# Performance work log

Measured on AMD Instinct MI355X. Metric: run time of the kernel, lower is better.

The kernel has to match this reference:

```python
import jax, jax.numpy as jnp
import numpy as np
from jax import lax

EPS = 1e-5

def _groupnorm1(v, scale, bias):
    # GroupNorm(1, C) on [bs, C] vectors (spatial dims are 1x1): normalize over C per sample
    m = jnp.mean(v, axis=-1, keepdims=True)
    var = jnp.mean((v - m) ** 2, axis=-1, keepdims=True)
    return (v - m) / jnp.sqrt(var + EPS) * scale + bias

def _mish(v):
    return v * jnp.tanh(jax.nn.softplus(v))


def setup_inputs() -> dict:
    key = jax.random.key(0)
    ks = jax.random.split(key, 5)
    bs, C, H, W = 32, 128, 64, 64
    K, red = 4, 16
    hid = C // red
    return {
        "x": jax.random.normal(ks[0], (bs, C, H, W), jnp.float32),
        "weight": jax.random.normal(ks[1], (K, C, C, 3, 3), jnp.float32) * 0.05,
        "bias": jax.random.normal(ks[2], (K, C), jnp.float32) * 0.05,
        "se_w1": jax.random.normal(ks[3], (hid, C), jnp.float32) * 0.1,
        "gn1_scale": jnp.ones((hid,), jnp.float32),
        "gn1_bias": jnp.zeros((hid,), jnp.float32),
        "se_w2": jax.random.normal(ks[4], (K, hid), jnp.float32) * 0.1,
        "gn2_scale": jnp.ones((K,), jnp.float32),
        "gn2_bias": jnp.zeros((K,), jnp.float32),
    }


def reference(x, weight, bias, se_w1, gn1_scale, gn1_bias, se_w2, gn2_scale, gn2_bias):
    bs, C, H, W = x.shape
    K, out_p, in_p, kh, kw = weight.shape

    # --- SqueezeAndExcitation attention -> [bs, K] in (0,1) ---
    pooled = jnp.mean(x, axis=(2, 3))                       # [bs, C]
    h1 = pooled @ se_w1.T                                   # [bs, hid] (1x1 conv, no bias)
    h1 = _mish(_groupnorm1(h1, gn1_scale, gn1_bias))
    h2 = h1 @ se_w2.T                                       # [bs, K]
    att = jax.nn.sigmoid(_groupnorm1(h2, gn2_scale, gn2_bias))

    # --- per-sample kernel / bias aggregation ---
    agg_w = jnp.einsum('bk,koihw->boihw', att, weight)      # [bs, out, in, kh, kw]
    agg_b = att @ bias                                      # [bs, out]

    # --- per-sample conv2d (equivalent to groups=bs grouped conv in torch) ---
    pad = ((1, 1), (1, 1))
    def per_sample(xi, wi):
        return lax.conv_general_dilated(
            xi[None], wi, window_strides=(1, 1), padding=pad,
            dimension_numbers=('NCHW', 'OIHW', 'NCHW'))[0]
    out = jax.vmap(per_sample)(x, agg_w)                    # [bs, out, H, W]
    return out + agg_b[:, :, None, None]
```

## Files before the change

kernel.cpp:

```cpp
#include <hip/hip_runtime.h>
#include <hip/hip_bf16.h>
#include <math.h>
#include <stdint.h>

#define EPS 1e-5f

typedef __attribute__((ext_vector_type(8))) short bf16x8;
typedef __attribute__((ext_vector_type(16))) float f32x16;

__device__ __forceinline__ ushort f2bf(float f) {
    union { float f; unsigned u; } v; v.f = f;
    unsigned r = (v.u + 0x7FFFu + ((v.u >> 16) & 1u)) >> 16;
    return (ushort)r;
}

__device__ __forceinline__ void dma16(const void* g, void* l) {
    __builtin_amdgcn_global_load_lds(
        (__attribute__((address_space(1))) const void*)(uintptr_t)g,
        (__attribute__((address_space(3))) void*)(uintptr_t)l,
        16, 0, 0);
}

__global__ __launch_bounds__(256) void transpose_kernel(const float* __restrict__ x,
                                                        ushort* __restrict__ xT,
                                                        float* __restrict__ pooled) {
    __shared__ float T[128][68];
    int bid = blockIdx.x;
    int b = (bid & 7) * 4 + (bid >> 9);
    int y = (bid >> 3) & 63;
    int t = threadIdx.x;

    int ic2 = t >> 1, half = t & 1;
    const float4* src = (const float4*)(x + (((size_t)b * 128 + ic2) * 64 + y) * 64 + half * 32);
    float4* trow = (float4*)&T[ic2][half * 32];
    float s = 0.f;
#pragma unroll
    for (int i = 0; i < 8; ++i) {
        float4 v = src[i];
        trow[i] = v;
        s += v.x + v.y + v.z + v.w;
    }
    s += __shfl_xor(s, 1, 64);
    if (half == 0) atomicAdd(&pooled[b * 128 + ic2], s * (1.0f / 4096.0f));
    __syncthreads();

    int col = t >> 2, icq = t & 3;
    uint pk[16];
#pragma unroll
    for (int jj = 0; jj < 16; ++jj) {
        float f0 = T[icq * 32 + 2 * jj][col];
        float f1 = T[icq * 32 + 2 * jj + 1][col];
        pk[jj] = (uint)f2bf(f0) | ((uint)f2bf(f1) << 16);
    }
    ushort* dst = xT + (((size_t)(b * 66 + y + 1)) * 66 + col + 1) * 128 + icq * 32;
    ((uint4*)dst)[0] = make_uint4(pk[0], pk[1], pk[2], pk[3]);
    ((uint4*)dst)[1] = make_uint4(pk[4], pk[5], pk[6], pk[7]);
    ((uint4*)dst)[2] = make_uint4(pk[8], pk[9], pk[10], pk[11]);
    ((uint4*)dst)[3] = make_uint4(pk[12], pk[13], pk[14], pk[15]);

    uint4 z = make_uint4(0, 0, 0, 0);
    if (y == 0) {
        uint4* row0 = (uint4*)(xT + ((size_t)b * 66 + 0) * 66 * 128);
        for (int i = t; i < 1056; i += 256) row0[i] = z;
    }
    if (y == 63) {
        uint4* row65 = (uint4*)(xT + ((size_t)b * 66 + 65) * 66 * 128);
        for (int i = t; i < 1056; i += 256) row65[i] = z;
    }
    if (t < 32) {
        int c = (t >> 4) * 65;
        int i = t & 15;
        *(uint4*)(xT + (((size_t)(b * 66 + y + 1)) * 66 + c) * 128 + i * 8) = z;
    }
}

__global__ __launch_bounds__(256) void aggw_kernel(const float* __restrict__ weight,
                                                   const float* __restrict__ pooled,
                                                   const float* __restrict__ se_w1,
                                                   const float* __restrict__ gn1_s, const float* __restrict__ gn1_b,
                                                   const float* __restrict__ se_w2,
                                                   const float* __restrict__ gn2_s, const float* __restrict__ gn2_b,
                                                   float* __restrict__ att_out,
                                                   ushort* __restrict__ aggw) {
    __shared__ float pl[8][128];
    __shared__ float h1s[8][8];
    __shared__ float att_s[8][4];
    int blk = blockIdx.x;
    int rep = blk / 72;
    int t = threadIdx.x;

#pragma unroll
    for (int u = 0; u < 4; ++u) {
        int pid = u * 256 + t;
        int bl = pid >> 7, ic = pid & 127;
        pl[bl][ic] = pooled[(rep * 8 + bl) * 128 + ic];
    }
    __syncthreads();
    if (t < 64) {
        int bl = t >> 3, jj = t & 7;
        float s1 = 0.f;
        for (int c = 0; c < 128; ++c) s1 += pl[bl][c] * se_w1[jj * 128 + c];
        h1s[bl][jj] = s1;
    }
    __syncthreads();
    if (t < 8) {
        float h1[8];
#pragma unroll
        for (int j = 0; j < 8; ++j) h1[j] = h1s[t][j];
        float m = 0.f;
#pragma unroll
        for (int j = 0; j < 8; ++j) m += h1[j];
        m *= 0.125f;
        float var = 0.f;
#pragma unroll
        for (int j = 0; j < 8; ++j) { float d = h1[j] - m; var += d * d; }
        var *= 0.125f;
        float inv = rsqrtf(var + EPS);
#pragma unroll
        for (int j = 0; j < 8; ++j) {
            float tt = (h1[j] - m) * inv * gn1_s[j] + gn1_b[j];
            float sp = (tt > 20.f) ? tt : log1pf(expf(tt));
            h1[j] = tt * tanhf(sp);
        }
        float h2[4];
#pragma unroll
        for (int k = 0; k < 4; ++k) {
            float s2 = 0.f;
#pragma unroll
            for (int j = 0; j < 8; ++j) s2 += h1[j] * se_w2[k * 8 + j];
            h2[k] = s2;
        }
        float m2 = 0.25f * (h2[0] + h2[1] + h2[2] + h2[3]);
        float v2 = 0.f;
#pragma unroll
        for (int k = 0; k < 4; ++k) { float d = h2[k] - m2; v2 += d * d; }
        v2 *= 0.25f;
        float inv2 = rsqrtf(v2 + EPS);
#pragma unroll
        for (int k = 0; k < 4; ++k) {
            float tt = (h2[k] - m2) * inv2 * gn2_s[k] + gn2_b[k];
            att_s[t][k] = 1.0f / (1.0f + expf(-tt));
        }
    }
    __syncthreads();

    if ((blk % 72) == 0 && t < 32) att_out[rep * 32 + t] = att_s[t >> 2][t & 3];

    int tq = (blk % 72) * 256 + t;
    int tap = tq >> 10;
    int within = tq & 1023;
    int oc = within >> 3;
    int p = within & 7;
    int g = (p - oc) & 7;
    int h = tap / 9, s = tap % 9;
    int ic0 = h * 64 + g * 8;

    float wv[4][8];
#pragma unroll
    for (int k = 0; k < 4; ++k)
#pragma unroll
        for (int j = 0; j < 8; ++j)
            wv[k][j] = weight[(((size_t)(k * 128 + oc)) * 128 + ic0 + j) * 9 + s];

#pragma unroll
    for (int bl = 0; bl < 8; ++bl) {
        int b = rep * 8 + bl;
        float a0 = att_s[bl][0], a1 = att_s[bl][1], a2 = att_s[bl][2], a3 = att_s[bl][3];
        uint pk[4];
#pragma unroll
        for (int q = 0; q < 4; ++q) {
            float f0 = a0 * wv[0][2 * q] + a1 * wv[1][2 * q] + a2 * wv[2][2 * q] + a3 * wv[3][2 * q];
            float f1 = a0 * wv[0][2 * q + 1] + a1 * wv[1][2 * q + 1] + a2 * wv[2][2 * q + 1] + a3 * wv[3][2 * q + 1];
            pk[q] = (uint)f2bf(f0) | ((uint)f2bf(f1) << 16);
        }
        *(uint4*)(aggw + (size_t)b * 147456 + (size_t)tq * 8) = make_uint4(pk[0], pk[1], pk[2], pk[3]);
    }
}

__global__ __launch_bounds__(256, 2) void conv_kernel(const ushort* __restrict__ xT,
                                                      const ushort* __restrict__ aggw,
                                                      const float* __restrict__ att,
                                                      const float* __restrict__ bias,
                                                      float* __restrict__ out) {
    __shared__ ushort ldsB[396 * 64];

    int bid = blockIdx.x;
    int xcd = bid & 7;
    int idx = bid >> 3;
    int b = xcd * 4 + (idx >> 4);
    int tile = idx & 15;
    int y0 = tile * 4;

    int tid = threadIdx.x;
    int l = tid & 63, w = tid >> 6;
    int wm = w >> 1, wn = w & 1;
    int l31 = l & 31, lhi = l >> 5;

    const ushort* xTb = xT + ((size_t)(b * 66 + y0)) * 66 * 128;
    const ushort* Asmp = aggw + (size_t)b * 147456;

    const ushort* ptrA[2];
    int rotA[2];
#pragma unroll
    for (int mi = 0; mi < 2; ++mi) {
        int oc = wm * 64 + mi * 32 + l31;
        ptrA[mi] = Asmp + oc * 64;
        rotA[mi] = (lhi + oc) & 7;
    }
    int CB[4];
#pragma unroll
    for (int nb = 0; nb < 4; ++nb) {
        int rs = nb >> 1, ch = nb & 1;
        CB[nb] = (2 * wn + rs) * 66 + ch * 32 + l31;
    }
    int rotB = (l31 + lhi) & 7;

    f32x16 acc[2][4];
#pragma unroll
    for (int mi = 0; mi < 2; ++mi)
#pragma unroll
        for (int nb = 0; nb < 4; ++nb)
#pragma unroll
            for (int q = 0; q < 16; ++q) acc[mi][nb][q] = 0.f;

    bf16x8 a[2][4];
#pragma unroll
    for (int mi = 0; mi < 2; ++mi)
#pragma unroll
        for (int icb = 0; icb < 4; ++icb)
            a[mi][icb] = *(const bf16x8*)(ptrA[mi] + (((rotA[mi] + 2 * icb) & 7) << 3));

#pragma unroll
    for (int i = 0; i < 13; ++i) {
        int k = i * 256 + tid;
        if (k < 3168) {
            int rc = k >> 3;
            int c = rc % 66;
            int g = ((k & 7) - c) & 7;
            dma16(xTb + (size_t)rc * 128 + (g << 3), &ldsB[(size_t)k * 8]);
        }
    }
    __syncthreads();

    for (int hs = 0; hs < 18; ++hs) {
        int s = (hs >= 9) ? hs - 9 : hs;
        int kh = s / 3, kw = s - kh * 3;
        int celladd = kh * 66 + kw;
        const ushort* Anext = Asmp + (size_t)(hs + 1) * 8192;
#pragma unroll
        for (int icb = 0; icb < 4; ++icb) {
            int slotb = (rotB + 2 * icb + kw) & 7;
            bf16x8 bb[4];
#pragma unroll
            for (int nb = 0; nb < 4; ++nb) {
                int cell = CB[nb] + celladd;
                bb[nb] = *(const bf16x8*)&ldsB[(cell << 6) + (slotb << 3)];
            }
#pragma unroll
            for (int mi = 0; mi < 2; ++mi)
#pragma unroll
                for (int nb = 0; nb < 4; ++nb)
                    acc[mi][nb] = __builtin_amdgcn_mfma_f32_32x32x16_bf16(a[mi][icb], bb[nb], acc[mi][nb], 0, 0, 0);
            if (hs < 17) {
#pragma unroll
                for (int mi = 0; mi < 2; ++mi) {
                    int oc64 = (wm * 64 + mi * 32 + l31) * 64;
                    a[mi][icb] = *(const bf16x8*)(Anext + oc64 + (((rotA[mi] + 2 * icb) & 7) << 3));
                }
            }
        }
        if (hs == 8) {
            __syncthreads();
#pragma unroll
            for (int i = 0; i < 13; ++i) {
                int k = i * 256 + tid;
                if (k < 3168) {
                    int rc = k >> 3;
                    int c = rc % 66;
                    int g = ((k & 7) - c) & 7;
                    dma16(xTb + (size_t)rc * 128 + 64 + (g << 3), &ldsB[(size_t)k * 8]);
                }
            }
            __syncthreads();
        }
    }

    float a0 = att[b * 4 + 0], a1 = att[b * 4 + 1], a2 = att[b * 4 + 2], a3 = att[b * 4 + 3];
#pragma unroll
    for (int mi = 0; mi < 2; ++mi)
#pragma unroll
        for (int q = 0; q < 16; ++q) {
            int oc = wm * 64 + mi * 32 + (q & 3) + 8 * (q >> 2) + 4 * lhi;
            float ab = a0 * bias[oc] + a1 * bias[128 + oc] + a2 * bias[256 + oc] + a3 * bias[384 + oc];
#pragma unroll
            for (int nb = 0; nb < 4; ++nb) {
                int y = y0 + 2 * wn + (nb >> 1);
                out[(((size_t)b * 128 + oc) * 64 + y) * 64 + (nb & 1) * 32 + l31] = acc[mi][nb][q] + ab;
            }
        }
}

extern "C" void kernel_launch(void* const* d_in, const int* in_sizes, int n_in,
                              void* d_out, int out_size, void* d_ws, size_t ws_size,
                              hipStream_t stream) {
    const float* x      = (const float*)d_in[0];
    const float* weight = (const float*)d_in[1];
    const float* bias   = (const float*)d_in[2];
    const float* se_w1  = (const float*)d_in[3];
    const float* gn1_s  = (const float*)d_in[4];
    const float* gn1_b  = (const float*)d_in[5];
    const float* se_w2  = (const float*)d_in[6];
    const float* gn2_s  = (const float*)d_in[7];
    const float* gn2_b  = (const float*)d_in[8];
    float* out = (float*)d_out;

    float*  att    = (float*)d_ws;
    float*  pooled = (float*)((char*)d_ws + 16384);
    ushort* aggw   = (ushort*)((char*)d_ws + 65536);
    ushort* xT     = (ushort*)((char*)d_ws + 10485760);

    hipMemsetAsync(pooled, 0, 128 * 32 * sizeof(float), stream);
    transpose_kernel<<<2048, 256, 0, stream>>>(x, xT, pooled);
    aggw_kernel<<<288, 256, 0, stream>>>(weight, pooled, se_w1, gn1_s, gn1_b,
                                         se_w2, gn2_s, gn2_b, att, aggw);
    conv_kernel<<<512, 256, 0, stream>>>(xT, aggw, att, bias, out);
}
```

Baseline: 91.36 us.

## Replace pooled atomics with per-row partial sums and relayout aggregated weights

The transpose kernel now writes per-row channel partial sums to a workspace buffer instead of issuing atomicAdds into a pooled array. This removes the memset launch and atomic contention, and the aggw kernel reduces the 64 partials per channel itself. The aggregated-weight layout also changes from a rotated per-oc swizzle to an [g][oc][8] layout, so conv kernel A-loads become simple coalesced offsets. In exchange the reduction adds a small extra buffer read in aggw and a changed load pattern in the transpose.

New measurement: 94.33 us. 1.03x slower.

```diff
diff --git a/kernel.cpp b/kernel.cpp
--- a/kernel.cpp
+++ b/kernel.cpp
@@ -23,25 +23,35 @@
 
 __global__ __launch_bounds__(256) void transpose_kernel(const float* __restrict__ x,
                                                         ushort* __restrict__ xT,
-                                                        float* __restrict__ pooled) {
+                                                        float* __restrict__ partial) {
     __shared__ float T[128][68];
     int bid = blockIdx.x;
     int b = (bid & 7) * 4 + (bid >> 9);
     int y = (bid >> 3) & 63;
     int t = threadIdx.x;
 
-    int ic2 = t >> 1, half = t & 1;
-    const float4* src = (const float4*)(x + (((size_t)b * 128 + ic2) * 64 + y) * 64 + half * 32);
-    float4* trow = (float4*)&T[ic2][half * 32];
-    float s = 0.f;
+    int g16 = t & 15;
+    int rsel = (t >> 4) & 3;
+    int wv = t >> 6;
+
+    float rs[8];
 #pragma unroll
     for (int i = 0; i < 8; ++i) {
-        float4 v = src[i];
-        trow[i] = v;
-        s += v.x + v.y + v.z + v.w;
-    }
-    s += __shfl_xor(s, 1, 64);
-    if (half == 0) atomicAdd(&pooled[b * 128 + ic2], s * (1.0f / 4096.0f));
+        int ic = wv * 32 + i * 4 + rsel;
+        float4 v = *(const float4*)(x + (((size_t)b * 128 + ic) * 64 + y) * 64 + g16 * 4);
+        *(float4*)&T[ic][g16 * 4] = v;
+        float sv = v.x + v.y + v.z + v.w;
+        sv += __shfl_xor(sv, 1, 64);
+        sv += __shfl_xor(sv, 2, 64);
+        sv += __shfl_xor(sv, 4, 64);
+        sv += __shfl_xor(sv, 8, 64);
+        rs[i] = sv;
+    }
+    if (g16 == 0) {
+#pragma unroll
+        for (int i = 0; i < 8; ++i)
+            partial[((size_t)b * 64 + y) * 128 + wv * 32 + i * 4 + rsel] = rs[i];
+    }
     __syncthreads();
 
     int col = t >> 2, icq = t & 3;
@@ -75,7 +85,7 @@
 }
 
 __global__ __launch_bounds__(256) void aggw_kernel(const float* __restrict__ weight,
-                                                   const float* __restrict__ pooled,
+                                                   const float* __restrict__ partial,
                                                    const float* __restrict__ se_w1,
                                                    const float* __restrict__ gn1_s, const float* __restrict__ gn1_b,
                                                    const float* __restrict__ se_w2,
@@ -93,7 +103,11 @@
     for (int u = 0; u < 4; ++u) {
         int pid = u * 256 + t;
         int bl = pid >> 7, ic = pid & 127;
-        pl[bl][ic] = pooled[(rep * 8 + bl) * 128 + ic];
+        const float* p = partial + ((size_t)(rep * 8 + bl) * 64) * 128 + ic;
+        float ssum = 0.f;
+#pragma unroll 8
+        for (int yy = 0; yy < 64; ++yy) ssum += p[yy * 128];
+        pl[bl][ic] = ssum * (1.0f / 4096.0f);
     }
     __syncthreads();
     if (t < 64) {
@@ -149,9 +163,8 @@
     int tq = (blk % 72) * 256 + t;
     int tap = tq >> 10;
     int within = tq & 1023;
-    int oc = within >> 3;
-    int p = within & 7;
-    int g = (p - oc) & 7;
+    int g = within >> 7;
+    int oc = within & 127;
     int h = tap / 9, s = tap % 9;
     int ic0 = h * 64 + g * 8;
 
@@ -199,13 +212,11 @@
     const ushort* xTb = xT + ((size_t)(b * 66 + y0)) * 66 * 128;
     const ushort* Asmp = aggw + (size_t)b * 147456;
 
-    const ushort* ptrA[2];
-    int rotA[2];
+    int ofsA[2];
 #pragma unroll
     for (int mi = 0; mi < 2; ++mi) {
         int oc = wm * 64 + mi * 32 + l31;
-        ptrA[mi] = Asmp + oc * 64;
-        rotA[mi] = (lhi + oc) & 7;
+        ofsA[mi] = (lhi * 128 + oc) * 8;
     }
     int CB[4];
 #pragma unroll
@@ -228,7 +239,7 @@
     for (int mi = 0; mi < 2; ++mi)
 #pragma unroll
         for (int icb = 0; icb < 4; ++icb)
-            a[mi][icb] = *(const bf16x8*)(ptrA[mi] + (((rotA[mi] + 2 * icb) & 7) << 3));
+            a[mi][icb] = *(const bf16x8*)(Asmp + ofsA[mi] + icb * 2048);
 
 #pragma unroll
     for (int i = 0; i < 13; ++i) {
@@ -263,10 +274,8 @@
                     acc[mi][nb] = __builtin_amdgcn_mfma_f32_32x32x16_bf16(a[mi][icb], bb[nb], acc[mi][nb], 0, 0, 0);
             if (hs < 17) {
 #pragma unroll
-                for (int mi = 0; mi < 2; ++mi) {
-                    int oc64 = (wm * 64 + mi * 32 + l31) * 64;
-                    a[mi][icb] = *(const bf16x8*)(Anext + oc64 + (((rotA[mi] + 2 * icb) & 7) << 3));
-                }
+                for (int mi = 0; mi < 2; ++mi)
+                    a[mi][icb] = *(const bf16x8*)(Anext + ofsA[mi] + icb * 2048);
             }
         }
         if (hs == 8) {
@@ -314,14 +323,13 @@
     const float* gn2_b  = (const float*)d_in[8];
     float* out = (float*)d_out;
 
-    float*  att    = (float*)d_ws;
-    float*  pooled = (float*)((char*)d_ws + 16384);
-    ushort* aggw   = (ushort*)((char*)d_ws + 65536);
-    ushort* xT     = (ushort*)((char*)d_ws + 10485760);
-
-    hipMemsetAsync(pooled, 0, 128 * 32 * sizeof(float), stream);
-    transpose_kernel<<<2048, 256, 0, stream>>>(x, xT, pooled);
-    aggw_kernel<<<288, 256, 0, stream>>>(weight, pooled, se_w1, gn1_s, gn1_b,
+    float*  att     = (float*)d_ws;
+    float*  partial = (float*)((char*)d_ws + 65536);
+    ushort* aggw    = (ushort*)((char*)d_ws + 1114112);
+    ushort* xT      = (ushort*)((char*)d_ws + 10551296);
+
+    transpose_kernel<<<2048, 256, 0, stream>>>(x, xT, partial);
+    aggw_kernel<<<288, 256, 0, stream>>>(weight, partial, se_w1, gn1_s, gn1_b,
                                          se_w2, gn2_s, gn2_b, att, aggw);
     conv_kernel<<<512, 256, 0, stream>>>(xT, aggw, att, bias, out);
 }
```
